# Performance work log

Hardware: AMD Instinct MI355X
Metric: run time of the kernel (lower is better)

The kernel has to match this reference:

```python
import jax, jax.numpy as jnp
import numpy as np

B, S, D_IN, HEAD_DIM = 4, 4096, 1024, 128

def setup_inputs() -> dict:
    key = jax.random.key(0)
    k1, k2, k3, k4 = jax.random.split(key, 4)
    x = jax.random.normal(k1, (B, S, D_IN), dtype=jnp.float32)
    # nn.Parameter(torch.rand(...)) -> uniform [0,1)
    W_query = jax.random.uniform(k2, (D_IN, HEAD_DIM), dtype=jnp.float32)
    W_key = jax.random.uniform(k3, (D_IN, HEAD_DIM), dtype=jnp.float32)
    W_value = jax.random.uniform(k4, (D_IN, HEAD_DIM), dtype=jnp.float32)
    return {"x": x, "W_query": W_query, "W_key": W_key, "W_value": W_value}

def reference(x, W_query, W_key, W_value):
    # x: [B,S,d_in]; W_*: [d_in,head_dim]
    queries = jnp.einsum('bsd,dh->bsh', x, W_query)
    keys = jnp.einsum('bsd,dh->bsh', x, W_key)
    values = jnp.einsum('bsd,dh->bsh', x, W_value)
    scale = 1.0 / jnp.sqrt(jnp.asarray(HEAD_DIM, dtype=x.dtype))
    attn_scores = jnp.einsum('bqh,bkh->bqk', queries, keys)  # [B,S,S]
    attn_weights = jax.nn.softmax(attn_scores * scale, axis=-1)
    context_vec = jnp.einsum('bqk,bkh->bqh', attn_weights, values)
    return context_vec
```

## Files before the change

### kernel.cpp

```cpp
#include <hip/hip_runtime.h>
#include <cstdint>

#define B_  4
#define S_  4096
#define DIN 1024
#define DH  128
#define SCALE 0.08838834764831845f

typedef short bf16x8 __attribute__((ext_vector_type(8)));
typedef float f32x4 __attribute__((ext_vector_type(4)));
typedef unsigned short u16;
typedef unsigned int   u32;

#define MFMA16(a, b, c) __builtin_amdgcn_mfma_f32_16x16x32_bf16(a, b, c, 0, 0, 0)

#define GLOAD_LDS16(g, l) __builtin_amdgcn_global_load_lds( \
    (const __attribute__((address_space(1))) void*)(g),     \
    (__attribute__((address_space(3))) void*)(l), 16, 0, 0)

__device__ inline u16 bf16_rn(float f) {
    union { float f; u32 u; } v; v.f = f;
    u32 r = v.u + 0x7FFFu + ((v.u >> 16) & 1u);
    return (u16)(r >> 16);
}
__device__ inline float bf16_f(u16 h) {
    union { u32 u; float f; } v; v.u = ((u32)h) << 16; return v.f;
}
__device__ inline u32 pk2(float a, float b) {
    return (u32)bf16_rn(a) | ((u32)bf16_rn(b) << 16);
}
__device__ inline void split2(float a, float b, u32& hi, u32& lo) {
    u32 ua = __builtin_bit_cast(u32, a), ub = __builtin_bit_cast(u32, b);
    u32 ha = ua & 0xFFFF0000u, hb = ub & 0xFFFF0000u;
    hi = (ua >> 16) | hb;
    float la = a - __builtin_bit_cast(float, ha);
    float lb = b - __builtin_bit_cast(float, hb);
    lo = (u32)bf16_rn(la) | ((u32)bf16_rn(lb) << 16);
}

__global__ __launch_bounds__(256) void wconv2(
    const float* __restrict__ Wq, const float* __restrict__ Wk, const float* __restrict__ Wv,
    u16* __restrict__ wpack)
{
    int id  = blockIdx.x * 256 + threadIdx.x;
    int s   = id / 2560;
    int rem = id % 2560;
    int p   = rem >> 9;
    int gi  = rem & 511;
    int n   = gi & 127, kq2 = gi >> 7;
    const float* W = (p < 2) ? Wq : (p < 4) ? Wk : Wv;
    int k0 = 32 * s + 8 * kq2;
    u16 o[8];
    #pragma unroll
    for (int j = 0; j < 8; ++j) {
        float v = W[(size_t)(k0 + j) * DH + n];
        if (p < 2) v *= SCALE;
        if (p == 4) {
            o[j] = bf16_rn(v);
        } else {
            u32 u = __builtin_bit_cast(u32, v);
            if ((p & 1) == 0) o[j] = (u16)(u >> 16);
            else o[j] = bf16_rn(v - __builtin_bit_cast(float, u & 0xFFFF0000u));
        }
    }
    u16* dst = wpack + (size_t)id * 8;
    *(uint4*)dst = *(uint4*)o;
}

__global__ __launch_bounds__(256) void qkv_v4(
    const float* __restrict__ x, const u16* __restrict__ wpack,
    u16* __restrict__ qhi, u16* __restrict__ qlo,
    u16* __restrict__ khi, u16* __restrict__ klo, u16* __restrict__ vt)
{
    __shared__ __align__(16) char lds[81920];

    const int t    = threadIdx.x;
    const int row0 = blockIdx.x * 64;
    const int lane = t & 63, wave = t >> 6;
    const int l15  = lane & 15, g = lane >> 4;
    const int wr   = wave >> 1, wc = wave & 1;

    f32x4 accq[2][4], acck[2][4], accv[2][4];
    #pragma unroll
    for (int rt = 0; rt < 2; ++rt)
        #pragma unroll
        for (int nt = 0; nt < 4; ++nt)
            #pragma unroll
            for (int r = 0; r < 4; ++r) {
                accq[rt][nt][r] = 0.f; acck[rt][nt][r] = 0.f; accv[rt][nt][r] = 0.f;
            }

    const char* WP = (const char*)wpack;
    auto stage = [&](int bufi, int s) {
        char* d = lds + bufi * 40960;
        const char* src = WP + (size_t)s * 40960;
        #pragma unroll
        for (int c = 0; c < 10; ++c) {
            int o = t * 16 + c * 4096;
            GLOAD_LDS16(src + o, d + o);
        }
    };

    const float* xp0 = x + (size_t)(row0 + 32 * wr + l15) * DIN + 8 * g;
    const float* xp1 = xp0 + (size_t)16 * DIN;

    float4 ca0 = *(const float4*)(xp0);
    float4 cb0 = *(const float4*)(xp0 + 4);
    float4 ca1 = *(const float4*)(xp1);
    float4 cb1 = *(const float4*)(xp1 + 4);

    stage(0, 0);
    __syncthreads();

    int buf = 0;
    for (int s = 0; s < 32; ++s) {
        if (s < 31) stage(buf ^ 1, s + 1);

        float4 na0, nb0, na1, nb1;
        if (s < 31) {
            na0 = *(const float4*)(xp0 + 32 * (s + 1));
            nb0 = *(const float4*)(xp0 + 32 * (s + 1) + 4);
            na1 = *(const float4*)(xp1 + 32 * (s + 1));
            nb1 = *(const float4*)(xp1 + 32 * (s + 1) + 4);
        }

        bf16x8 xh[2], xl[2];
        {
            uint4 H, L;
            split2(ca0.x, ca0.y, H.x, L.x); split2(ca0.z, ca0.w, H.y, L.y);
            split2(cb0.x, cb0.y, H.z, L.z); split2(cb0.z, cb0.w, H.w, L.w);
            xh[0] = __builtin_bit_cast(bf16x8, H);
            xl[0] = __builtin_bit_cast(bf16x8, L);
        }
        {
            uint4 H, L;
            split2(ca1.x, ca1.y, H.x, L.x); split2(ca1.z, ca1.w, H.y, L.y);
            split2(cb1.x, cb1.y, H.z, L.z); split2(cb1.z, cb1.w, H.w, L.w);
            xh[1] = __builtin_bit_cast(bf16x8, H);
            xl[1] = __builtin_bit_cast(bf16x8, L);
        }

        const char* wb = lds + buf * 40960;
        #pragma unroll
        for (int nt = 0; nt < 4; ++nt) {
            const int n  = 64 * wc + 16 * nt + l15;
            const int wo = (g << 11) + (n << 4);
            bf16x8 qwh = *(const bf16x8*)(wb + wo);
            bf16x8 qwl = *(const bf16x8*)(wb +  8192 + wo);
            bf16x8 kwh = *(const bf16x8*)(wb + 16384 + wo);
            bf16x8 kwl = *(const bf16x8*)(wb + 24576 + wo);
            bf16x8 vwh = *(const bf16x8*)(wb + 32768 + wo);
            #pragma unroll
            for (int rt = 0; rt < 2; ++rt) {
                accq[rt][nt] = MFMA16(xh[rt], qwh, accq[rt][nt]);
                accq[rt][nt] = MFMA16(xl[rt], qwh, accq[rt][nt]);
                accq[rt][nt] = MFMA16(xh[rt], qwl, accq[rt][nt]);
                acck[rt][nt] = MFMA16(xh[rt], kwh, acck[rt][nt]);
                acck[rt][nt] = MFMA16(xl[rt], kwh, acck[rt][nt]);
                acck[rt][nt] = MFMA16(xh[rt], kwl, acck[rt][nt]);
                accv[rt][nt] = MFMA16(xh[rt], vwh, accv[rt][nt]);
            }
        }
        __syncthreads();
        if (s < 31) { ca0 = na0; cb0 = nb0; ca1 = na1; cb1 = nb1; }
        buf ^= 1;
    }

    #pragma unroll
    for (int rt = 0; rt < 2; ++rt) {
        #pragma unroll
        for (int reg = 0; reg < 4; ++reg) {
            int r  = row0 + 32 * wr + 16 * rt + 4 * g + reg;
            int bb = r >> 12, sr = r & 4095, kt = sr >> 6, kr = sr & 63;
            #pragma unroll
            for (int nt = 0; nt < 4; ++nt) {
                int c = 64 * wc + 16 * nt + l15;
                {
                    float v = accq[rt][nt][reg];
                    u32 u = __builtin_bit_cast(u32, v);
                    float lo = v - __builtin_bit_cast(float, u & 0xFFFF0000u);
                    size_t o = (size_t)r * DH + c;
                    qhi[o] = (u16)(u >> 16);
                    qlo[o] = bf16_rn(lo);
                }
                {
                    float v = acck[rt][nt][reg];
                    u32 u = __builtin_bit_cast(u32, v);
                    float lo = v - __builtin_bit_cast(float, u & 0xFFFF0000u);
                    size_t o = ((size_t)(bb * 64 + kt) * 64 + kr) * 128
                             + (((c >> 3) ^ (kr & 15)) << 3) + (c & 7);
                    khi[o] = (u16)(u >> 16);
                    klo[o] = bf16_rn(lo);
                }
                {
                    float v = accv[rt][nt][reg];
                    size_t o = ((size_t)(bb * 64 + kt) * 128 + c) * 64
                             + (((kr >> 3) ^ (c & 7)) << 3) + (kr & 7);
                    vt[o] = bf16_rn(v);
                }
            }
        }
    }
}

__global__ __launch_bounds__(512, 2) void flash4(
    const u16* __restrict__ qhi, const u16* __restrict__ qlo,
    const u16* __restrict__ khi, const u16* __restrict__ klo,
    const u16* __restrict__ vt,
    u16* __restrict__ opart, float2* __restrict__ ml)
{
    __shared__ __align__(16) char smem[2 * 49152];

    const int tid  = threadIdx.x;
    const int wave = tid >> 6, lane = tid & 63;
    const int l15  = lane & 15, g = lane >> 4;
    const int bid  = blockIdx.x;
    const int pair = bid & 15, qt = bid >> 4;
    const int b = pair >> 2, z = pair & 3;

    const int q0row = b * S_ + qt * 256 + wave * 32;

    bf16x8 qh[2][4], ql[2][4];
    #pragma unroll
    for (int h = 0; h < 2; ++h)
        #pragma unroll
        for (int ks = 0; ks < 4; ++ks) {
            size_t qa = (size_t)(q0row + 16 * h + l15) * DH + 32 * ks + 8 * g;
            qh[h][ks] = *(const bf16x8*)(qhi + qa);
            ql[h][ks] = *(const bf16x8*)(qlo + qa);
        }

    f32x4 O0[8], O1[8];
    #pragma unroll
    for (int dt = 0; dt < 8; ++dt)
        #pragma unroll
        for (int r = 0; r < 4; ++r) { O0[dt][r] = 0.f; O1[dt][r] = 0.f; }

    float m0 = -3.0e38f, l0 = 0.f, m1 = -3.0e38f, l1 = 0.f;

    int koff[4];
    #pragma unroll
    for (int ks = 0; ks < 4; ++ks)
        koff[ks] = (((4 * ks + g) ^ l15) << 4) + (l15 << 8);
    int voff[2];
    #pragma unroll
    for (int kw = 0; kw < 2; ++kw)
        voff[kw] = (((4 * kw + g) ^ (l15 & 7)) << 4);

    const char* kbase = (const char*)(khi + (size_t)b * 64 * 8192);
    const char* lbase = (const char*)(klo + (size_t)b * 64 * 8192);
    const char* vbase = (const char*)(vt  + (size_t)b * 64 * 8192);
    const int kt0 = z * 16;

    auto stage = [&](int bufi, int ktl) {
        const char* sk = kbase + (size_t)(kt0 + ktl) * 16384;
        const char* sl = lbase + (size_t)(kt0 + ktl) * 16384;
        const char* sv = vbase + (size_t)(kt0 + ktl) * 16384;
        char* dk = smem + bufi * 49152;
        #pragma unroll
        for (int c = 0; c < 2; ++c) {
            int o = tid * 16 + c * 8192;
            GLOAD_LDS16(sk + o, dk + o);
            GLOAD_LDS16(sl + o, dk + 16384 + o);
            GLOAD_LDS16(sv + o, dk + 32768 + o);
        }
    };

    stage(0, 0);
    __syncthreads();

    int buf = 0;
    for (int ktl = 0; ktl < 16; ++ktl) {
        if (ktl < 15) stage(buf ^ 1, ktl + 1);

        const char* bk = smem + buf * 49152;
        const char* bl = bk + 16384;
        const char* bv = bk + 32768;

        f32x4 s0[4], s1[4];
        #pragma unroll
        for (int nt = 0; nt < 4; ++nt)
            #pragma unroll
            for (int r = 0; r < 4; ++r) { s0[nt][r] = 0.f; s1[nt][r] = 0.f; }

        #pragma unroll
        for (int ks = 0; ks < 4; ++ks) {
            #pragma unroll
            for (int nt = 0; nt < 4; ++nt) {
                bf16x8 kh = *(const bf16x8*)(bk + nt * 4096 + koff[ks]);
                bf16x8 kl = *(const bf16x8*)(bl + nt * 4096 + koff[ks]);
                s0[nt] = MFMA16(kh, qh[0][ks], s0[nt]);
                s0[nt] = MFMA16(kh, ql[0][ks], s0[nt]);
                s0[nt] = MFMA16(kl, qh[0][ks], s0[nt]);
                s1[nt] = MFMA16(kh, qh[1][ks], s1[nt]);
                s1[nt] = MFMA16(kh, ql[1][ks], s1[nt]);
                s1[nt] = MFMA16(kl, qh[1][ks], s1[nt]);
            }
        }

        u32 pk0[4][2], pk1[4][2];
        float fsc0, fsc1;
        {
            float mloc = -3.0e38f;
            #pragma unroll
            for (int nt = 0; nt < 4; ++nt)
                #pragma unroll
                for (int r = 0; r < 4; ++r) mloc = fmaxf(mloc, s0[nt][r]);
            mloc = fmaxf(mloc, __shfl_xor(mloc, 16));
            mloc = fmaxf(mloc, __shfl_xor(mloc, 32));
            float mnew = fmaxf(m0, mloc);
            fsc0 = __expf(m0 - mnew);
            m0 = mnew;
            float ps = 0.f;
            #pragma unroll
            for (int nt = 0; nt < 4; ++nt) {
                float p0 = __expf(s0[nt][0] - mnew);
                float p1 = __expf(s0[nt][1] - mnew);
                float p2 = __expf(s0[nt][2] - mnew);
                float p3 = __expf(s0[nt][3] - mnew);
                ps += (p0 + p1) + (p2 + p3);
                pk0[nt][0] = pk2(p0, p1);
                pk0[nt][1] = pk2(p2, p3);
            }
            ps += __shfl_xor(ps, 16);
            ps += __shfl_xor(ps, 32);
            l0 = l0 * fsc0 + ps;
        }
        {
            float mloc = -3.0e38f;
            #pragma unroll
            for (int nt = 0; nt < 4; ++nt)
                #pragma unroll
                for (int r = 0; r < 4; ++r) mloc = fmaxf(mloc, s1[nt][r]);
            mloc = fmaxf(mloc, __shfl_xor(mloc, 16));
            mloc = fmaxf(mloc, __shfl_xor(mloc, 32));
            float mnew = fmaxf(m1, mloc);
            fsc1 = __expf(m1 - mnew);
            m1 = mnew;
            float ps = 0.f;
            #pragma unroll
            for (int nt = 0; nt < 4; ++nt) {
                float p0 = __expf(s1[nt][0] - mnew);
                float p1 = __expf(s1[nt][1] - mnew);
                float p2 = __expf(s1[nt][2] - mnew);
                float p3 = __expf(s1[nt][3] - mnew);
                ps += (p0 + p1) + (p2 + p3);
                pk1[nt][0] = pk2(p0, p1);
                pk1[nt][1] = pk2(p2, p3);
            }
            ps += __shfl_xor(ps, 16);
            ps += __shfl_xor(ps, 32);
            l1 = l1 * fsc1 + ps;
        }

        float fr0[4], fr1[4];
        #pragma unroll
        for (int r = 0; r < 4; ++r) {
            fr0[r] = __shfl(fsc0, 4 * g + r);
            fr1[r] = __shfl(fsc1, 4 * g + r);
        }
        #pragma unroll
        for (int dt = 0; dt < 8; ++dt)
            #pragma unroll
            for (int r = 0; r < 4; ++r) {
                O0[dt][r] *= fr0[r];
                O1[dt][r] *= fr1[r];
            }

        const int s0l = l15 | ((2 * (g & 1)) << 4);
        const int s1l = s0l + 16;
        const int hiH = g >> 1;
        #pragma unroll
        for (int kw = 0; kw < 2; ++kw) {
            u32 a0, a1, a2, a3, c0, c1, c2, c3;
            {
                u32 x0 = __shfl(pk0[2 * kw][0], s0l), y0 = __shfl(pk0[2 * kw + 1][0], s0l);
                u32 x1 = __shfl(pk0[2 * kw][1], s0l), y1 = __shfl(pk0[2 * kw + 1][1], s0l);
                u32 x2 = __shfl(pk0[2 * kw][0], s1l), y2 = __shfl(pk0[2 * kw + 1][0], s1l);
                u32 x3 = __shfl(pk0[2 * kw][1], s1l), y3 = __shfl(pk0[2 * kw + 1][1], s1l);
                a0 = hiH ? y0 : x0; a1 = hiH ? y1 : x1;
                a2 = hiH ? y2 : x2; a3 = hiH ? y3 : x3;
            }
            {
                u32 x0 = __shfl(pk1[2 * kw][0], s0l), y0 = __shfl(pk1[2 * kw + 1][0], s0l);
                u32 x1 = __shfl(pk1[2 * kw][1], s0l), y1 = __shfl(pk1[2 * kw + 1][1], s0l);
                u32 x2 = __shfl(pk1[2 * kw][0], s1l), y2 = __shfl(pk1[2 * kw + 1][0], s1l);
                u32 x3 = __shfl(pk1[2 * kw][1], s1l), y3 = __shfl(pk1[2 * kw + 1][1], s1l);
                c0 = hiH ? y0 : x0; c1 = hiH ? y1 : x1;
                c2 = hiH ? y2 : x2; c3 = hiH ? y3 : x3;
            }
            union { u32 w[4]; bf16x8 v; } pa, pb;
            pa.w[0] = a0; pa.w[1] = a1; pa.w[2] = a2; pa.w[3] = a3;
            pb.w[0] = c0; pb.w[1] = c1; pb.w[2] = c2; pb.w[3] = c3;
            #pragma unroll
            for (int dt = 0; dt < 8; ++dt) {
                bf16x8 vf = *(const bf16x8*)(bv + (16 * dt + l15) * 128 + voff[kw]);
                O0[dt] = MFMA16(pa.v, vf, O0[dt]);
                O1[dt] = MFMA16(pb.v, vf, O1[dt]);
            }
        }

        __syncthreads();
        buf ^= 1;
    }

    u16* op = opart + ((size_t)z * 16384 + q0row) * DH;
    #pragma unroll
    for (int dt = 0; dt < 8; ++dt)
        #pragma unroll
        for (int r = 0; r < 4; ++r) {
            op[(size_t)(4 * g + r) * DH + 16 * dt + l15]      = bf16_rn(O0[dt][r]);
            op[(size_t)(16 + 4 * g + r) * DH + 16 * dt + l15] = bf16_rn(O1[dt][r]);
        }
    if (lane < 16) {
        ml[(size_t)z * 16384 + q0row + lane]      = make_float2(m0, l0);
        ml[(size_t)z * 16384 + q0row + 16 + lane] = make_float2(m1, l1);
    }
}

__global__ __launch_bounds__(256) void merge4(
    const u16* __restrict__ op, const float2* __restrict__ ml, float* __restrict__ O)
{
    int row = blockIdx.x * 16 + (threadIdx.x >> 4);
    int dq  = (threadIdx.x & 15) * 8;
    float2 a[4];
    #pragma unroll
    for (int zz = 0; zz < 4; ++zz) a[zz] = ml[(size_t)zz * 16384 + row];
    float M = fmaxf(fmaxf(a[0].x, a[1].x), fmaxf(a[2].x, a[3].x));
    float w[4], den = 0.f;
    #pragma unroll
    for (int zz = 0; zz < 4; ++zz) {
        w[zz] = __expf(a[zz].x - M);
        den += a[zz].y * w[zz];
    }
    float inv = 1.0f / den;
    float acc[8];
    #pragma unroll
    for (int j = 0; j < 8; ++j) acc[j] = 0.f;
    #pragma unroll
    for (int zz = 0; zz < 4; ++zz) {
        const u16* p = op + ((size_t)zz * 16384 + row) * DH + dq;
        bf16x8 vv = *(const bf16x8*)p;
        #pragma unroll
        for (int j = 0; j < 8; ++j) acc[j] += w[zz] * bf16_f((u16)vv[j]);
    }
    float4 oa, ob;
    oa.x = acc[0] * inv; oa.y = acc[1] * inv; oa.z = acc[2] * inv; oa.w = acc[3] * inv;
    ob.x = acc[4] * inv; ob.y = acc[5] * inv; ob.z = acc[6] * inv; ob.w = acc[7] * inv;
    *(float4*)(O + (size_t)row * DH + dq)     = oa;
    *(float4*)(O + (size_t)row * DH + dq + 4) = ob;
}

extern "C" void kernel_launch(void* const* d_in, const int* in_sizes, int n_in,
                              void* d_out, int out_size, void* d_ws, size_t ws_size,
                              hipStream_t stream) {
    const float* x  = (const float*)d_in[0];
    const float* Wq = (const float*)d_in[1];
    const float* Wk = (const float*)d_in[2];
    const float* Wv = (const float*)d_in[3];
    float* out = (float*)d_out;

    const size_t SZ = (size_t)B_ * S_ * DH;
    u16* qhi = (u16*)d_ws;
    u16* qlo = qhi + SZ;
    u16* khi = qlo + SZ;
    u16* klo = khi + SZ;
    u16* vtp = klo + SZ;
    u16* wpk = vtp + SZ;
    u16*    opart = (u16*)((char*)wpk + 1310720);
    float2* mlp   = (float2*)((char*)opart + (size_t)4 * 16384 * 128 * 2);

    wconv2<<<320, 256, 0, stream>>>(Wq, Wk, Wv, wpk);
    qkv_v4<<<256, 256, 0, stream>>>(x, wpk, qhi, qlo, khi, klo, vtp);
    flash4<<<256, 512, 0, stream>>>(qhi, qlo, khi, klo, vtp, opart, mlp);
    merge4<<<1024, 256, 0, stream>>>(opart, mlp, out);
}
```

Before: 151.7 us.

## Split keys 8-way, single-buffer LDS for occupancy, exp2 with lazy rescale

```diff
diff --git a/kernel.cpp b/kernel.cpp
--- a/kernel.cpp
+++ b/kernel.cpp
@@ -5,7 +5,7 @@
 #define S_  4096
 #define DIN 1024
 #define DH  128
-#define SCALE 0.08838834764831845f
+#define QSCALE (0.08838834764831845f * 1.4426950408889634f)
 
 typedef short bf16x8 __attribute__((ext_vector_type(8)));
 typedef float f32x4 __attribute__((ext_vector_type(4)));
@@ -17,6 +17,12 @@
 #define GLOAD_LDS16(g, l) __builtin_amdgcn_global_load_lds( \
     (const __attribute__((address_space(1))) void*)(g),     \
     (__attribute__((address_space(3))) void*)(l), 16, 0, 0)
+
+#if __has_builtin(__builtin_amdgcn_exp2f)
+#define EXP2(x) __builtin_amdgcn_exp2f(x)
+#else
+#define EXP2(x) exp2f(x)
+#endif
 
 __device__ inline u16 bf16_rn(float f) {
     union { float f; u32 u; } v; v.f = f;
@@ -54,7 +60,7 @@
     #pragma unroll
     for (int j = 0; j < 8; ++j) {
         float v = W[(size_t)(k0 + j) * DH + n];
-        if (p < 2) v *= SCALE;
+        if (p < 2) v *= QSCALE;
         if (p == 4) {
             o[j] = bf16_rn(v);
         } else {
@@ -203,20 +209,23 @@
     }
 }
 
-__global__ __launch_bounds__(512, 2) void flash4(
+template <int Z>
+__global__ __launch_bounds__(512, 4) void flash8(
     const u16* __restrict__ qhi, const u16* __restrict__ qlo,
     const u16* __restrict__ khi, const u16* __restrict__ klo,
     const u16* __restrict__ vt,
     u16* __restrict__ opart, float2* __restrict__ ml)
 {
-    __shared__ __align__(16) char smem[2 * 49152];
+    __shared__ __align__(16) char smem[49152];
+    constexpr int TILES = 64 / Z;
 
     const int tid  = threadIdx.x;
     const int wave = tid >> 6, lane = tid & 63;
     const int l15  = lane & 15, g = lane >> 4;
     const int bid  = blockIdx.x;
-    const int pair = bid & 15, qt = bid >> 4;
-    const int b = pair >> 2, z = pair & 3;
+    const int grp  = bid & (4 * Z - 1);
+    const int qt   = bid / (4 * Z);
+    const int b    = grp / Z, z = grp % Z;
 
     const int q0row = b * S_ + qt * 256 + wave * 32;
 
@@ -250,30 +259,26 @@
     const char* kbase = (const char*)(khi + (size_t)b * 64 * 8192);
     const char* lbase = (const char*)(klo + (size_t)b * 64 * 8192);
     const char* vbase = (const char*)(vt  + (size_t)b * 64 * 8192);
-    const int kt0 = z * 16;
-
-    auto stage = [&](int bufi, int ktl) {
+    const int kt0 = z * TILES;
+
+    auto stage = [&](int ktl) {
         const char* sk = kbase + (size_t)(kt0 + ktl) * 16384;
         const char* sl = lbase + (size_t)(kt0 + ktl) * 16384;
         const char* sv = vbase + (size_t)(kt0 + ktl) * 16384;
-        char* dk = smem + bufi * 49152;
         #pragma unroll
         for (int c = 0; c < 2; ++c) {
             int o = tid * 16 + c * 8192;
-            GLOAD_LDS16(sk + o, dk + o);
-            GLOAD_LDS16(sl + o, dk + 16384 + o);
-            GLOAD_LDS16(sv + o, dk + 32768 + o);
+            GLOAD_LDS16(sk + o, smem + o);
+            GLOAD_LDS16(sl + o, smem + 16384 + o);
+            GLOAD_LDS16(sv + o, smem + 32768 + o);
         }
     };
 
-    stage(0, 0);
-    __syncthreads();
-
-    int buf = 0;
-    for (int ktl = 0; ktl < 16; ++ktl) {
-        if (ktl < 15) stage(buf ^ 1, ktl + 1);
-
-        const char* bk = smem + buf * 49152;
+    for (int ktl = 0; ktl < TILES; ++ktl) {
+        stage(ktl);
+        __syncthreads();
+
+        const char* bk = smem;
         const char* bl = bk + 16384;
         const char* bv = bk + 32768;
 
@@ -298,74 +303,59 @@
             }
         }
 
+        float ml0 = -3.0e38f, ml1 = -3.0e38f;
+        #pragma unroll
+        for (int nt = 0; nt < 4; ++nt)
+            #pragma unroll
+            for (int r = 0; r < 4; ++r) {
+                ml0 = fmaxf(ml0, s0[nt][r]);
+                ml1 = fmaxf(ml1, s1[nt][r]);
+            }
+        ml0 = fmaxf(ml0, __shfl_xor(ml0, 16));
+        ml0 = fmaxf(ml0, __shfl_xor(ml0, 32));
+        ml1 = fmaxf(ml1, __shfl_xor(ml1, 16));
+        ml1 = fmaxf(ml1, __shfl_xor(ml1, 32));
+
+        if (!__all((ml0 <= m0 + 8.0f) & (ml1 <= m1 + 8.0f))) {
+            float mn0 = fmaxf(m0, ml0), mn1 = fmaxf(m1, ml1);
+            float fsc0 = EXP2(m0 - mn0), fsc1 = EXP2(m1 - mn1);
+            m0 = mn0; m1 = mn1;
+            l0 *= fsc0; l1 *= fsc1;
+            float fr0[4], fr1[4];
+            #pragma unroll
+            for (int r = 0; r < 4; ++r) {
+                fr0[r] = __shfl(fsc0, 4 * g + r);
+                fr1[r] = __shfl(fsc1, 4 * g + r);
+            }
+            #pragma unroll
+            for (int dt = 0; dt < 8; ++dt)
+                #pragma unroll
+                for (int r = 0; r < 4; ++r) {
+                    O0[dt][r] *= fr0[r];
+                    O1[dt][r] *= fr1[r];
+                }
+        }
+
         u32 pk0[4][2], pk1[4][2];
-        float fsc0, fsc1;
-        {
-            float mloc = -3.0e38f;
-            #pragma unroll
-            for (int nt = 0; nt < 4; ++nt)
-                #pragma unroll
-                for (int r = 0; r < 4; ++r) mloc = fmaxf(mloc, s0[nt][r]);
-            mloc = fmaxf(mloc, __shfl_xor(mloc, 16));
-            mloc = fmaxf(mloc, __shfl_xor(mloc, 32));
-            float mnew = fmaxf(m0, mloc);
-            fsc0 = __expf(m0 - mnew);
-            m0 = mnew;
-            float ps = 0.f;
-            #pragma unroll
-            for (int nt = 0; nt < 4; ++nt) {
-                float p0 = __expf(s0[nt][0] - mnew);
-                float p1 = __expf(s0[nt][1] - mnew);
-                float p2 = __expf(s0[nt][2] - mnew);
-                float p3 = __expf(s0[nt][3] - mnew);
-                ps += (p0 + p1) + (p2 + p3);
-                pk0[nt][0] = pk2(p0, p1);
-                pk0[nt][1] = pk2(p2, p3);
-            }
-            ps += __shfl_xor(ps, 16);
-            ps += __shfl_xor(ps, 32);
-            l0 = l0 * fsc0 + ps;
-        }
-        {
-            float mloc = -3.0e38f;
-            #pragma unroll
-            for (int nt = 0; nt < 4; ++nt)
-                #pragma unroll
-                for (int r = 0; r < 4; ++r) mloc = fmaxf(mloc, s1[nt][r]);
-            mloc = fmaxf(mloc, __shfl_xor(mloc, 16));
-            mloc = fmaxf(mloc, __shfl_xor(mloc, 32));
-            float mnew = fmaxf(m1, mloc);
-            fsc1 = __expf(m1 - mnew);
-            m1 = mnew;
-            float ps = 0.f;
-            #pragma unroll
-            for (int nt = 0; nt < 4; ++nt) {
-                float p0 = __expf(s1[nt][0] - mnew);
-                float p1 = __expf(s1[nt][1] - mnew);
-                float p2 = __expf(s1[nt][2] - mnew);
-                float p3 = __expf(s1[nt][3] - mnew);
-                ps += (p0 + p1) + (p2 + p3);
-                pk1[nt][0] = pk2(p0, p1);
-                pk1[nt][1] = pk2(p2, p3);
-            }
-            ps += __shfl_xor(ps, 16);
-            ps += __shfl_xor(ps, 32);
-            l1 = l1 * fsc1 + ps;
-        }
-
-        float fr0[4], fr1[4];
-        #pragma unroll
-        for (int r = 0; r < 4; ++r) {
-            fr0[r] = __shfl(fsc0, 4 * g + r);
-            fr1[r] = __shfl(fsc1, 4 * g + r);
-        }
-        #pragma unroll
-        for (int dt = 0; dt < 8; ++dt)
-            #pragma unroll
-            for (int r = 0; r < 4; ++r) {
-                O0[dt][r] *= fr0[r];
-                O1[dt][r] *= fr1[r];
-            }
+        float ps0 = 0.f, ps1 = 0.f;
+        #pragma unroll
+        for (int nt = 0; nt < 4; ++nt) {
+            float a0 = EXP2(s0[nt][0] - m0), a1 = EXP2(s0[nt][1] - m0);
+            float a2 = EXP2(s0[nt][2] - m0), a3 = EXP2(s0[nt][3] - m0);
+            ps0 += (a0 + a1) + (a2 + a3);
+            pk0[nt][0] = pk2(a0, a1);
+            pk0[nt][1] = pk2(a2, a3);
+            float c0 = EXP2(s1[nt][0] - m1), c1 = EXP2(s1[nt][1] - m1);
+            float c2 = EXP2(s1[nt][2] - m1), c3 = EXP2(s1[nt][3] - m1);
+            ps1 += (c0 + c1) + (c2 + c3);
+            pk1[nt][0] = pk2(c0, c1);
+            pk1[nt][1] = pk2(c2, c3);
+        }
+        ps0 += __shfl_xor(ps0, 16);
+        ps0 += __shfl_xor(ps0, 32);
+        ps1 += __shfl_xor(ps1, 16);
+        ps1 += __shfl_xor(ps1, 32);
+        l0 += ps0; l1 += ps1;
 
         const int s0l = l15 | ((2 * (g & 1)) << 4);
         const int s1l = s0l + 16;
@@ -401,7 +391,6 @@
         }
 
         __syncthreads();
-        buf ^= 1;
     }
 
     u16* op = opart + ((size_t)z * 16384 + q0row) * DH;
@@ -418,19 +407,22 @@
     }
 }
 
-__global__ __launch_bounds__(256) void merge4(
+template <int NZ>
+__global__ __launch_bounds__(256) void mergeZ(
     const u16* __restrict__ op, const float2* __restrict__ ml, float* __restrict__ O)
 {
     int row = blockIdx.x * 16 + (threadIdx.x >> 4);
     int dq  = (threadIdx.x & 15) * 8;
-    float2 a[4];
-    #pragma unroll
-    for (int zz = 0; zz < 4; ++zz) a[zz] = ml[(size_t)zz * 16384 + row];
-    float M = fmaxf(fmaxf(a[0].x, a[1].x), fmaxf(a[2].x, a[3].x));
-    float w[4], den = 0.f;
-    #pragma unroll
-    for (int zz = 0; zz < 4; ++zz) {
-        w[zz] = __expf(a[zz].x - M);
+    float2 a[NZ];
+    #pragma unroll
+    for (int zz = 0; zz < NZ; ++zz) a[zz] = ml[(size_t)zz * 16384 + row];
+    float M = a[0].x;
+    #pragma unroll
+    for (int zz = 1; zz < NZ; ++zz) M = fmaxf(M, a[zz].x);
+    float w[NZ], den = 0.f;
+    #pragma unroll
+    for (int zz = 0; zz < NZ; ++zz) {
+        w[zz] = EXP2(a[zz].x - M);
         den += a[zz].y * w[zz];
     }
     float inv = 1.0f / den;
@@ -438,7 +430,7 @@
     #pragma unroll
     for (int j = 0; j < 8; ++j) acc[j] = 0.f;
     #pragma unroll
-    for (int zz = 0; zz < 4; ++zz) {
+    for (int zz = 0; zz < NZ; ++zz) {
         const u16* p = op + ((size_t)zz * 16384 + row) * DH + dq;
         bf16x8 vv = *(const bf16x8*)p;
         #pragma unroll
@@ -467,11 +459,19 @@
     u16* klo = khi + SZ;
     u16* vtp = klo + SZ;
     u16* wpk = vtp + SZ;
-    u16*    opart = (u16*)((char*)wpk + 1310720);
-    float2* mlp   = (float2*)((char*)opart + (size_t)4 * 16384 * 128 * 2);
+    u16* opart = wpk + 655360;
+    size_t head = (size_t)((char*)opart - (char*)d_ws);
+    size_t need8 = head + (size_t)8 * 16384 * DH * 2 + (size_t)8 * 16384 * 8;
 
     wconv2<<<320, 256, 0, stream>>>(Wq, Wk, Wv, wpk);
     qkv_v4<<<256, 256, 0, stream>>>(x, wpk, qhi, qlo, khi, klo, vtp);
-    flash4<<<256, 512, 0, stream>>>(qhi, qlo, khi, klo, vtp, opart, mlp);
-    merge4<<<1024, 256, 0, stream>>>(opart, mlp, out);
-}
+    if (ws_size >= need8) {
+        float2* mlp = (float2*)((char*)opart + (size_t)8 * 16384 * DH * 2);
+        flash8<8><<<512, 512, 0, stream>>>(qhi, qlo, khi, klo, vtp, opart, mlp);
+        mergeZ<8><<<1024, 256, 0, stream>>>(opart, mlp, out);
+    } else {
+        float2* mlp = (float2*)((char*)opart + (size_t)4 * 16384 * DH * 2);
+        flash8<4><<<256, 512, 0, stream>>>(qhi, qlo, khi, klo, vtp, opart, mlp);
+        mergeZ<4><<<1024, 256, 0, stream>>>(opart, mlp, out);
+    }
+}
```

Measured after the change: 259.1 us. 70.9% more time.
